# Kernel tuning notes

Hardware: AMD Instinct MI355X
Metric: run time of the kernel (lower is better)

## Reference

```python
import jax, jax.numpy as jnp
from jax import lax
import numpy as np

N = 17          # num_joints
HID = 64        # hidden_dim
EPS = 1e-5      # BatchNorm eps
SKELETON_CONNECTIONS = [(0, 1), (0, 2), (1, 3), (2, 4), (5, 7), (7, 9), (6, 8), (8, 10), (5, 6), (5, 11), (6, 12), (11, 13), (13, 15), (12, 14), (14, 16), (11, 12)]


def _build_adj():
    a = np.zeros((N, N), dtype=np.float32)
    np.fill_diagonal(a, 1.0)
    for i, j in SKELETON_CONNECTIONS:
        a[i, j] = 1.0
        a[j, i] = 1.0
    dinv = 1.0 / np.sqrt(a.sum(1))
    return jnp.asarray(a * dinv[:, None] * dinv[None, :])

ADJ = _build_adj()  # [N, N], D^-1/2 (A+I) D^-1/2


def _bn(x, g, b):
    # eval-mode BatchNorm1d with running_mean=0, running_var=1; x: [B, C, T]
    s = g / jnp.sqrt(1.0 + EPS)
    return x * s[None, :, None] + b[None, :, None]


def _gconv1d(x, w, b, groups, pad):
    # grouped temporal conv; x: [B, C, T], w: [Cout, Cin//groups, K]
    y = lax.conv_general_dilated(x, w, (1,), [(pad, pad)], feature_group_count=groups,
                                 dimension_numbers=('NCH', 'OIH', 'NCH'))
    return y + b[None, :, None]


def _block(x, gw, gb, bn1g, bn1b, cw, cb, bn2g, bn2b, res):
    # STGCNBlock; x: [B, T, N, Cin]
    B, T, n, Cin = x.shape
    Cout = gw.shape[1]
    xr = x.reshape(B, T, n * Cin).transpose(0, 2, 1)  # [B, n*Cin, T]
    if res is None:
        r = xr
    else:
        rw, rb, rg, rbb = res
        r = _bn(_gconv1d(xr, rw, rb, n, 0), rg, rbb)
    # GCN applied to all timesteps at once (replaces the per-t python loop):
    # support = x @ W ; out = adj @ support + bias
    y = jnp.einsum('mn,btno->btmo', ADJ, jnp.einsum('btni,io->btno', x, gw)) + gb
    h = y.reshape(B, T, n * Cout).transpose(0, 2, 1)  # [B, n*Cout, T]
    h = jax.nn.relu(_bn(h, bn1g, bn1b))
    h = _gconv1d(h, cw, cb, n, 1)                    # k=3, pad=1, groups=N
    h = jax.nn.relu(_bn(h, bn2g, bn2b))              # dropout is identity (eval)
    out = h + r
    return out.transpose(0, 2, 1).reshape(B, T, n, Cout)


def setup_inputs() -> dict:
    key = jax.random.key(0)
    ks = iter(jax.random.split(key, 64))

    def rn(shape, scale=0.05):
        return (scale * jax.random.normal(next(ks), shape)).astype(jnp.float32)

    B, T = 64, 512
    C = 2 * HID  # 128
    inp = {'x': jax.random.normal(next(ks), (B, T, N * 3), dtype=jnp.float32)}
    inp['w_in'] = rn((HID, 3))
    inp['b_in'] = rn((HID,))
    for i, cin in enumerate([HID, C, C]):
        inp[f'gw{i}'] = rn((cin, C))
        inp[f'gb{i}'] = rn((C,))
        inp[f'bn1g{i}'] = 1.0 + rn((N * C,))
        inp[f'bn1b{i}'] = rn((N * C,))
        inp[f'cw{i}'] = rn((N * C, C, 3))
        inp[f'cb{i}'] = rn((N * C,))
        inp[f'bn2g{i}'] = 1.0 + rn((N * C,))
        inp[f'bn2b{i}'] = rn((N * C,))
    inp['rw0'] = rn((N * C, HID, 1))
    inp['rb0'] = rn((N * C,))
    inp['rg0'] = 1.0 + rn((N * C,))
    inp['rbb0'] = rn((N * C,))
    inp['w1'] = rn((N * C, 128))
    inp['b1'] = rn((128,))
    inp['w2'] = rn((128, 64))
    inp['b2'] = rn((64,))
    inp['w3'] = rn((64, 1))
    inp['b3'] = rn((1,))
    return inp


def reference(x, w_in, b_in, gw0, gb0, bn1g0, bn1b0, cw0, cb0, bn2g0, bn2b0,
              gw1, gb1, bn1g1, bn1b1, cw1, cb1, bn2g1, bn2b1,
              gw2, gb2, bn1g2, bn1b2, cw2, cb2, bn2g2, bn2b2,
              rw0, rb0, rg0, rbb0, w1, b1, w2, b2, w3, b3):
    B, T, F = x.shape
    x4 = x.reshape(B, T, N, F // N)                       # [B,T,N,3]
    h = jnp.einsum('btnc,oc->btno', x4, w_in) + b_in      # Conv1d k=1 input transform
    h = _block(h, gw0, gb0, bn1g0, bn1b0, cw0, cb0, bn2g0, bn2b0, (rw0, rb0, rg0, rbb0))
    h = _block(h, gw1, gb1, bn1g1, bn1b1, cw1, cb1, bn2g1, bn2b1, None)
    h = _block(h, gw2, gb2, bn1g2, bn1b2, cw2, cb2, bn2g2, bn2b2, None)
    h = h.mean(axis=1).reshape(B, -1)                     # temporal mean -> [B, N*2*HID]
    h = jax.nn.relu(h @ w1 + b1)
    h = jax.nn.relu(h @ w2 + b2)
    return jax.nn.sigmoid(h @ w3 + b3)                    # [B, 1]
```

## Files before the change

kernel.cpp:

```cpp
#include <hip/hip_runtime.h>
#include <math.h>

#define BNUM 64
#define TNUM 512
#define NJ   17
#define CC   128
#define HIDC 64

#define RSQ 0.9999950000374997f

typedef __attribute__((ext_vector_type(8))) short bf16x8;
typedef __attribute__((ext_vector_type(4))) float f32x4;

__device__ __forceinline__ float bf2f(unsigned short u) {
    union { unsigned int i; float f; } v; v.i = ((unsigned int)u) << 16; return v.f;
}
__device__ __forceinline__ unsigned short f2bf(float f) {
    union { float f; unsigned int i; } v; v.f = f;
    return (unsigned short)((v.i + 0x7FFF + ((v.i >> 16) & 1)) >> 16);
}
__device__ __forceinline__ void unpack8(const uint4 v, float* f) {
    f[0] = bf2f((unsigned short)(v.x & 0xFFFF)); f[1] = bf2f((unsigned short)(v.x >> 16));
    f[2] = bf2f((unsigned short)(v.y & 0xFFFF)); f[3] = bf2f((unsigned short)(v.y >> 16));
    f[4] = bf2f((unsigned short)(v.z & 0xFFFF)); f[5] = bf2f((unsigned short)(v.z >> 16));
    f[6] = bf2f((unsigned short)(v.w & 0xFFFF)); f[7] = bf2f((unsigned short)(v.w >> 16));
}
__device__ __forceinline__ uint4 pack8(const float* f) {
    uint4 v;
    v.x = (unsigned)f2bf(f[0]) | ((unsigned)f2bf(f[1]) << 16);
    v.y = (unsigned)f2bf(f[2]) | ((unsigned)f2bf(f[3]) << 16);
    v.z = (unsigned)f2bf(f[4]) | ((unsigned)f2bf(f[5]) << 16);
    v.w = (unsigned)f2bf(f[6]) | ((unsigned)f2bf(f[7]) << 16);
    return v;
}

constexpr unsigned ADJM[NJ] = {
    0x7u, 0xBu, 0x15u, 0xAu, 0x14u,
    0x8E0u, 0x1160u, 0x2A0u, 0x540u, 0x280u, 0x500u,
    0x3820u, 0x5840u, 0xA800u, 0x15000u, 0xA000u, 0x14000u
};
constexpr float DINV[NJ] = {
    0.5773502691896258f, 0.5773502691896258f, 0.5773502691896258f,
    0.7071067811865476f, 0.7071067811865476f,
    0.5f, 0.5f,
    0.5773502691896258f, 0.5773502691896258f,
    0.7071067811865476f, 0.7071067811865476f,
    0.5f, 0.5f,
    0.5773502691896258f, 0.5773502691896258f,
    0.7071067811865476f, 0.7071067811865476f
};

__global__ void k_fallback(float* out) { out[threadIdx.x] = 0.f; }
__global__ void k_zero(float* p, int n) {
    const int i = blockIdx.x * 256 + threadIdx.x;
    if (i < n) p[i] = 0.f;
}

__global__ void k_prep_cwB(const float* __restrict__ cw0, const float* __restrict__ cw1,
                           const float* __restrict__ cw2, unsigned short* __restrict__ cwB) {
    const int idx = blockIdx.x * 256 + threadIdx.x;
    if (idx >= NJ * CC * 3 * CC) return;
    const float* cw = (blockIdx.y == 0) ? cw0 : (blockIdx.y == 1) ? cw1 : cw2;
    const int oc = idx / 384, kk = idx % 384;
    const int ktap = kk >> 7, i = kk & 127;
    cwB[(size_t)blockIdx.y * (NJ * CC * 3 * CC) + idx] =
        f2bf(cw[((size_t)oc * CC + i) * 3 + ktap]);
}
__global__ void k_prep_rwB(const float* __restrict__ rw, unsigned short* __restrict__ rwB) {
    const int idx = blockIdx.x * 256 + threadIdx.x;
    if (idx >= NJ * CC * HIDC) return;
    rwB[idx] = f2bf(rw[idx]);
}
template<int CIN>
__global__ void k_prep_gwB(const float* __restrict__ gw, unsigned short* __restrict__ gwB) {
    const int idx = blockIdx.x * 256 + threadIdx.x;
    if (idx >= CC * CIN) return;
    const int o = idx / CIN, i = idx % CIN;
    gwB[idx] = f2bf(gw[i * CC + o]);
}

template<int CIN>
__device__ __forceinline__ void gcn_mfma_body(
        const unsigned short* __restrict__ gwB,
        const float* __restrict__ gb,
        const float* __restrict__ bn1g, const float* __restrict__ bn1b,
        unsigned short* __restrict__ H1, unsigned short* lds,
        int bt0, int tid) {
    const int lane = tid & 63;
    const int wnt  = tid >> 6;
    const int rbase = lane & 15;
    const int g8    = (lane >> 4) * 8;

    f32x4 acc[17][2] = {};
#pragma unroll
    for (int ks = 0; ks < CIN / 32; ++ks) {
        bf16x8 bfr[2];
#pragma unroll
        for (int nt = 0; nt < 2; ++nt)
            bfr[nt] = *reinterpret_cast<const bf16x8*>(
                &gwB[(size_t)(wnt * 32 + nt * 16 + rbase) * CIN + ks * 32 + g8]);
#pragma unroll
        for (int mt = 0; mt < 17; ++mt) {
            const int rl = mt * 16 + rbase;
            const bf16x8 a = *reinterpret_cast<const bf16x8*>(
                &lds[(rl * CIN + ks * 32 + g8) ^ ((rl & 7) << 3)]);
            acc[mt][0] = __builtin_amdgcn_mfma_f32_16x16x32_bf16(a, bfr[0], acc[mt][0], 0, 0, 0);
            acc[mt][1] = __builtin_amdgcn_mfma_f32_16x16x32_bf16(a, bfr[1], acc[mt][1], 0, 0, 0);
        }
    }
    __syncthreads();

    const int rrow = (lane >> 4) * 4;
#pragma unroll
    for (int mt = 0; mt < 17; ++mt)
#pragma unroll
        for (int nt = 0; nt < 2; ++nt)
#pragma unroll
            for (int q = 0; q < 4; ++q) {
                const int r = mt * 16 + rrow + q;
                const int o = wnt * 32 + nt * 16 + rbase;
                lds[(r * 128 + o) ^ ((r & 7) << 3)] = f2bf(acc[mt][nt][q]);
            }
    __syncthreads();

    const int btl = tid >> 4;
    const int cg  = tid & 15;
    float s8[NJ][8];
#pragma unroll
    for (int n = 0; n < NJ; ++n) {
        const int r = btl * NJ + n;
        const uint4 raw = *reinterpret_cast<const uint4*>(
            &lds[(r * 128 + cg * 8) ^ ((r & 7) << 3)]);
        unpack8(raw, s8[n]);
    }
#pragma unroll
    for (int m = 0; m < NJ; ++m) {
        float ym[8] = {};
#pragma unroll
        for (int n = 0; n < NJ; ++n) {
            if (ADJM[m] & (1u << n)) {
#pragma unroll
                for (int j = 0; j < 8; ++j) ym[j] = fmaf(s8[n][j], DINV[n], ym[j]);
            }
        }
        const int ch0 = m * CC + cg * 8;
        const float4 g0 = *reinterpret_cast<const float4*>(&gb[ch0]);
        const float4 g1 = *reinterpret_cast<const float4*>(&gb[ch0 + 4]);
        const float4 a0 = *reinterpret_cast<const float4*>(&bn1g[ch0]);
        const float4 a1 = *reinterpret_cast<const float4*>(&bn1g[ch0 + 4]);
        const float4 c0 = *reinterpret_cast<const float4*>(&bn1b[ch0]);
        const float4 c1 = *reinterpret_cast<const float4*>(&bn1b[ch0 + 4]);
        const float gbv[8] = {g0.x, g0.y, g0.z, g0.w, g1.x, g1.y, g1.z, g1.w};
        const float sgv[8] = {a0.x, a0.y, a0.z, a0.w, a1.x, a1.y, a1.z, a1.w};
        const float sbv[8] = {c0.x, c0.y, c0.z, c0.w, c1.x, c1.y, c1.z, c1.w};
        float out8[8];
#pragma unroll
        for (int j = 0; j < 8; ++j) {
            const float y = fmaf(ym[j], DINV[m], gbv[j]);
            out8[j] = fmaxf(fmaf(y, sgv[j] * RSQ, sbv[j]), 0.f);
        }
        *reinterpret_cast<uint4*>(&H1[(size_t)(bt0 + btl) * (NJ * CC) + ch0]) = pack8(out8);
    }
}

__global__ __launch_bounds__(256, 1) void k_gcn_mfma(
        const unsigned short* __restrict__ X, const unsigned short* __restrict__ gwB,
        const float* __restrict__ gb,
        const float* __restrict__ bn1g, const float* __restrict__ bn1b,
        unsigned short* __restrict__ H1) {
    __shared__ __align__(16) unsigned short lds[272 * 128];
    const int bt0 = blockIdx.x * 16;
    const int tid = threadIdx.x;
    for (int c = tid; c < 272 * 16; c += 256) {
        const int rl = c >> 4, s8 = c & 15;
        const uint4 v = *reinterpret_cast<const uint4*>(
            &X[(size_t)(bt0 * NJ + rl) * CC + s8 * 8]);
        *reinterpret_cast<uint4*>(&lds[(rl * 128 + s8 * 8) ^ ((rl & 7) << 3)]) = v;
    }
    __syncthreads();
    gcn_mfma_body<CC>(gwB, gb, bn1g, bn1b, H1, lds, bt0, tid);
}

__global__ __launch_bounds__(256, 1) void k_gcn0_mfma(
        const float* __restrict__ x,
        const float* __restrict__ w_in, const float* __restrict__ b_in,
        const unsigned short* __restrict__ gwB,
        const float* __restrict__ gb,
        const float* __restrict__ bn1g, const float* __restrict__ bn1b,
        unsigned short* __restrict__ H1) {
    __shared__ __align__(16) unsigned short lds[272 * 128];
    const int bt0 = blockIdx.x * 16;
    const int tid = threadIdx.x;
    for (int c = tid; c < 272 * 8; c += 256) {
        const int rl = c >> 3, i8 = c & 7;
        const int bt = bt0 + rl / NJ, n = rl % NJ;
        const float* xb = &x[(size_t)bt * (NJ * 3) + n * 3];
        const float x0 = xb[0], x1 = xb[1], x2 = xb[2];
        unsigned short tmp[8];
#pragma unroll
        for (int jj = 0; jj < 8; ++jj) {
            const int i = i8 * 8 + jj;
            tmp[jj] = f2bf(fmaf(x2, w_in[i * 3 + 2],
                           fmaf(x1, w_in[i * 3 + 1],
                           fmaf(x0, w_in[i * 3 + 0], b_in[i]))));
        }
        *reinterpret_cast<uint4*>(&lds[(rl * HIDC + i8 * 8) ^ ((rl & 7) << 3)]) =
            *reinterpret_cast<uint4*>(tmp);
    }
    __syncthreads();
    gcn_mfma_body<HIDC>(gwB, gb, bn1g, bn1b, H1, lds, bt0, tid);
}

template<int RES_MODE, int POOL>
__global__ __launch_bounds__(256) void k_tconv_mfma(
        const unsigned short* __restrict__ H1, const unsigned short* __restrict__ cwB,
        const float* __restrict__ cb,
        const float* __restrict__ bn2g, const float* __restrict__ bn2b,
        const float* __restrict__ RSRC,
        const float* __restrict__ w_in, const float* __restrict__ b_in,
        const unsigned short* __restrict__ rwB, const float* __restrict__ rb,
        const float* __restrict__ rg, const float* __restrict__ rbb,
        unsigned short* __restrict__ OUT, float* __restrict__ pooled) {
    __shared__ __align__(16) unsigned short xin[66 * 128];
    __shared__ __align__(16) unsigned short h0s[RES_MODE ? 64 * 64 : 8];

    const int t0  = blockIdx.x * 64;
    const int n   = blockIdx.y;
    const int b   = blockIdx.z;
    const int tid = threadIdx.x;
    const int lane = tid & 63;
    const int wnt  = tid >> 6;

    for (int c = tid; c < 66 * 16; c += 256) {
        const int row = c >> 4, slot = c & 15;
        const int ti = t0 - 1 + row;
        uint4 v = {0u, 0u, 0u, 0u};
        if (ti >= 0 && ti < TNUM)
            v = *reinterpret_cast<const uint4*>(
                    &H1[(((size_t)b * TNUM + ti) * NJ + n) * CC + slot * 8]);
        const int u = (row * 128 + slot * 8) ^ ((row & 7) << 3);
        *reinterpret_cast<uint4*>(&xin[u]) = v;
    }
    if constexpr (RES_MODE == 1) {
        for (int c = tid; c < 64 * 8; c += 256) {
            const int r = c >> 3, i8 = c & 7;
            const float* xb = &RSRC[((size_t)b * TNUM + t0 + r) * (NJ * 3) + n * 3];
            const float x0 = xb[0], x1 = xb[1], x2 = xb[2];
            unsigned short tmp[8];
#pragma unroll
            for (int j = 0; j < 8; ++j) {
                const int i = i8 * 8 + j;
                tmp[j] = f2bf(fmaf(x2, w_in[i * 3 + 2],
                              fmaf(x1, w_in[i * 3 + 1],
                              fmaf(x0, w_in[i * 3 + 0], b_in[i]))));
            }
            const int u = (r * 64 + i8 * 8) ^ ((r & 7) << 3);
            *reinterpret_cast<uint4*>(&h0s[u]) = *reinterpret_cast<uint4*>(tmp);
        }
    }
    __syncthreads();

    const int rbase = lane & 15;
    const int g8    = (lane >> 4) * 8;

    f32x4 acc[4][2] = {};
    for (int ks = 0; ks < 12; ++ks) {
        const int ktap = ks >> 2;
        const int ib   = (ks & 3) * 32 + g8;
        bf16x8 a[4];
#pragma unroll
        for (int m = 0; m < 4; ++m) {
            const int rl = m * 16 + rbase + ktap;
            a[m] = *reinterpret_cast<const bf16x8*>(
                       &xin[(rl * 128 + ib) ^ ((rl & 7) << 3)]);
        }
#pragma unroll
        for (int nt = 0; nt < 2; ++nt) {
            const int o = wnt * 32 + nt * 16 + rbase;
            const bf16x8 bf = *reinterpret_cast<const bf16x8*>(
                &cwB[(size_t)(n * CC + o) * 384 + ks * 32 + g8]);
#pragma unroll
            for (int m = 0; m < 4; ++m)
                acc[m][nt] = __builtin_amdgcn_mfma_f32_16x16x32_bf16(a[m], bf, acc[m][nt], 0, 0, 0);
        }
    }

    f32x4 accr[4][2] = {};
    if constexpr (RES_MODE == 1) {
        for (int ks = 0; ks < 2; ++ks) {
            const int ib = ks * 32 + g8;
            bf16x8 a[4];
#pragma unroll
            for (int m = 0; m < 4; ++m) {
                const int rl = m * 16 + rbase;
                a[m] = *reinterpret_cast<const bf16x8*>(
                           &h0s[(rl * 64 + ib) ^ ((rl & 7) << 3)]);
            }
#pragma unroll
            for (int nt = 0; nt < 2; ++nt) {
                const int o = wnt * 32 + nt * 16 + rbase;
                const bf16x8 bf = *reinterpret_cast<const bf16x8*>(
                    &rwB[(size_t)(n * CC + o) * HIDC + ib]);
#pragma unroll
                for (int m = 0; m < 4; ++m)
                    accr[m][nt] = __builtin_amdgcn_mfma_f32_16x16x32_bf16(a[m], bf, accr[m][nt], 0, 0, 0);
            }
        }
    }

    __syncthreads();

    const int rrow = (lane >> 4) * 4;
#pragma unroll
    for (int nt = 0; nt < 2; ++nt) {
        const int o  = wnt * 32 + nt * 16 + rbase;
        const int ch = n * CC + o;
        const float s2 = bn2g[ch] * RSQ, bb2 = bn2b[ch], cbo = cb[ch];
        float rs = 0.f, rsh = 0.f, rbc = 0.f;
        if constexpr (RES_MODE == 1) { rs = rg[ch] * RSQ; rsh = rbb[ch]; rbc = rb[ch]; }
#pragma unroll
        for (int m = 0; m < 4; ++m) {
#pragma unroll
            for (int q = 0; q < 4; ++q) {
                const int r = m * 16 + rrow + q;
                float v = fmaxf(fmaf(acc[m][nt][q] + cbo, s2, bb2), 0.f);
                if constexpr (RES_MODE == 1) v += fmaf(accr[m][nt][q] + rbc, rs, rsh);
                xin[(r * 128 + o) ^ ((r & 7) << 3)] = f2bf(v);
            }
        }
    }
    __syncthreads();

    float pacc[8] = {};
    for (int c = tid; c < 64 * 16; c += 256) {
        const int r = c >> 4, s8 = c & 15;
        uint4 v = *reinterpret_cast<const uint4*>(
            &xin[(r * 128 + s8 * 8) ^ ((r & 7) << 3)]);
        const size_t oi = (((size_t)b * TNUM + t0 + r) * NJ + n) * CC + s8 * 8;
        if constexpr (RES_MODE == 0) {
            float f[8], g[8];
            unpack8(v, f);
            unpack8(*reinterpret_cast<const uint4*>(&OUT[oi]), g);
#pragma unroll
            for (int j = 0; j < 8; ++j) f[j] += g[j];
            if constexpr (POOL == 1) {
#pragma unroll
                for (int j = 0; j < 8; ++j) pacc[j] += f[j];
            } else {
                *reinterpret_cast<uint4*>(&OUT[oi]) = pack8(f);
            }
        } else {
            *reinterpret_cast<uint4*>(&OUT[oi]) = v;
        }
    }

    if constexpr (POOL == 1) {
        __syncthreads();
        float* fred = reinterpret_cast<float*>(xin);
#pragma unroll
        for (int j = 0; j < 8; ++j) fred[tid * 8 + j] = pacc[j];
        __syncthreads();
        if (tid < 128) {
            const int s8 = tid >> 3, j = tid & 7;
            float s = 0.f;
#pragma unroll
            for (int k = 0; k < 16; ++k) s += fred[(s8 + 16 * k) * 8 + j];
            atomicAdd(&pooled[((size_t)b * NJ + n) * CC + s8 * 8 + j], s * (1.0f / TNUM));
        }
    }
}

__global__ __launch_bounds__(128) void k_mlp(const float* __restrict__ P,
        const float* __restrict__ w1, const float* __restrict__ b1,
        const float* __restrict__ w2, const float* __restrict__ b2,
        const float* __restrict__ w3, const float* __restrict__ b3,
        float* __restrict__ out) {
    __shared__ float h1[128];
    __shared__ float h2[64];
    const int b = blockIdx.x, tid = threadIdx.x;
    const float* pr = P + (size_t)b * (NJ * CC);
    float acc = b1[tid];
    for (int i = 0; i < NJ * CC; ++i) acc = fmaf(pr[i], w1[i * 128 + tid], acc);
    h1[tid] = fmaxf(acc, 0.f);
    __syncthreads();
    if (tid < 64) {
        float a2 = b2[tid];
#pragma unroll 4
        for (int i = 0; i < 128; ++i) a2 = fmaf(h1[i], w2[i * 64 + tid], a2);
        h2[tid] = fmaxf(a2, 0.f);
    }
    __syncthreads();
    if (tid == 0) {
        float a3 = b3[0];
#pragma unroll 4
        for (int i = 0; i < 64; ++i) a3 = fmaf(h2[i], w3[i], a3);
        out[b] = 1.f / (1.f + expf(-a3));
    }
}

extern "C" void kernel_launch(void* const* d_in, const int* in_sizes, int n_in,
                              void* d_out, int out_size, void* d_ws, size_t ws_size,
                              hipStream_t stream) {
    const float* x    = (const float*)d_in[0];
    const float* w_in = (const float*)d_in[1];
    const float* b_in = (const float*)d_in[2];
    const float *gw[3], *gb[3], *bn1g[3], *bn1b[3], *cw[3], *cb[3], *bn2g[3], *bn2b[3];
    for (int l = 0; l < 3; ++l) {
        const int base = 3 + l * 8;
        gw[l]   = (const float*)d_in[base + 0];
        gb[l]   = (const float*)d_in[base + 1];
        bn1g[l] = (const float*)d_in[base + 2];
        bn1b[l] = (const float*)d_in[base + 3];
        cw[l]   = (const float*)d_in[base + 4];
        cb[l]   = (const float*)d_in[base + 5];
        bn2g[l] = (const float*)d_in[base + 6];
        bn2b[l] = (const float*)d_in[base + 7];
    }
    const float* rw0  = (const float*)d_in[27];
    const float* rb0  = (const float*)d_in[28];
    const float* rg0  = (const float*)d_in[29];
    const float* rbb0 = (const float*)d_in[30];
    const float* w1   = (const float*)d_in[31];
    const float* b1   = (const float*)d_in[32];
    const float* w2   = (const float*)d_in[33];
    const float* b2   = (const float*)d_in[34];
    const float* w3   = (const float*)d_in[35];
    const float* b3   = (const float*)d_in[36];

    const size_t CWB    = (size_t)NJ * CC * 3 * CC;
    const size_t RWB    = (size_t)NJ * CC * HIDC;
    const size_t GWB128 = (size_t)CC * CC;
    const size_t GWB64  = (size_t)CC * HIDC;
    const size_t ACT_B  = (size_t)TNUM * NJ * CC;
    const size_t POOLED = (size_t)BNUM * NJ * CC;
    const size_t fixedB = (3 * CWB + RWB + 2 * GWB128 + GWB64) * sizeof(unsigned short)
                        + POOLED * sizeof(float);

    int chunk = 0;
    for (int c = BNUM; c >= 1; c >>= 1) {
        const size_t need = fixedB + 2 * (size_t)c * ACT_B * sizeof(unsigned short);
        if (need <= ws_size) { chunk = c; break; }
    }
    if (chunk == 0) {
        k_fallback<<<1, 64, 0, stream>>>((float*)d_out);
        return;
    }

    unsigned short* cwB0 = (unsigned short*)d_ws;
    unsigned short* cwB1 = cwB0 + CWB;
    unsigned short* cwB2 = cwB1 + CWB;
    unsigned short* rwB  = cwB2 + CWB;
    unsigned short* gwB0 = rwB + RWB;
    unsigned short* gwB1 = gwB0 + GWB64;
    unsigned short* gwB2 = gwB1 + GWB128;
    float* pooled = (float*)(gwB2 + GWB128);
    unsigned short* bufA = (unsigned short*)(pooled + POOLED);
    unsigned short* bufB = bufA + (size_t)chunk * ACT_B;

    dim3 pgrid((int)((CWB + 255) / 256), 3, 1);
    k_prep_cwB<<<pgrid, 256, 0, stream>>>(cw[0], cw[1], cw[2], cwB0);
    k_prep_rwB<<<(int)((RWB + 255) / 256), 256, 0, stream>>>(rw0, rwB);
    k_prep_gwB<HIDC><<<(int)((GWB64 + 255) / 256), 256, 0, stream>>>(gw[0], gwB0);
    k_prep_gwB<CC><<<(int)((GWB128 + 255) / 256), 256, 0, stream>>>(gw[1], gwB1);
    k_prep_gwB<CC><<<(int)((GWB128 + 255) / 256), 256, 0, stream>>>(gw[2], gwB2);
    k_zero<<<(int)((POOLED + 255) / 256), 256, 0, stream>>>(pooled, (int)POOLED);

    for (int b0 = 0; b0 < BNUM; b0 += chunk) {
        const float* xc = x + (size_t)b0 * TNUM * NJ * 3;
        const int GB = chunk * TNUM / 16;
        const dim3 tgrid(TNUM / 64, NJ, chunk);
        float* pc = pooled + (size_t)b0 * NJ * CC;

        k_gcn0_mfma<<<GB, 256, 0, stream>>>(xc, w_in, b_in, gwB0,
                                            gb[0], bn1g[0], bn1b[0], bufA);
        k_tconv_mfma<1, 0><<<tgrid, 256, 0, stream>>>(bufA, cwB0, cb[0], bn2g[0], bn2b[0],
                                                      xc, w_in, b_in, rwB, rb0, rg0, rbb0,
                                                      bufB, nullptr);
        k_gcn_mfma<<<GB, 256, 0, stream>>>(bufB, gwB1, gb[1], bn1g[1], bn1b[1], bufA);
        k_tconv_mfma<0, 0><<<tgrid, 256, 0, stream>>>(bufA, cwB1, cb[1], bn2g[1], bn2b[1],
                                                      nullptr, w_in, b_in, nullptr, nullptr, nullptr, nullptr,
                                                      bufB, nullptr);
        k_gcn_mfma<<<GB, 256, 0, stream>>>(bufB, gwB2, gb[2], bn1g[2], bn1b[2], bufA);
        k_tconv_mfma<0, 1><<<tgrid, 256, 0, stream>>>(bufA, cwB2, cb[2], bn2g[2], bn2b[2],
                                                      nullptr, w_in, b_in, nullptr, nullptr, nullptr, nullptr,
                                                      bufB, pc);
    }

    k_mlp<<<BNUM, 128, 0, stream>>>(pooled, w1, b1, w2, b2, w3, b3, (float*)d_out);
}
```

Before: 1.038 ms.

## Loop temporal conv blocks over time with double-buffered LDS prefetch

The temporal conv kernel now launches one block per (joint, batch) and loops over all eight 64-step time tiles. The next tile is prefetched into registers and written to a second LDS buffer, which overlaps global loads with MFMA work. The epilogue writes output straight from accumulators instead of staging through LDS. Pooling now reduces in registers with wave shuffles and a plain store, so the atomics and the zeroing kernel go away. The weight-prep kernels are merged into one launch. Grid parallelism drops eightfold (17×chunk blocks), which risks low occupancy, and the element-wise bf16 global stores are less coalesced.

```diff
diff --git a/kernel.cpp b/kernel.cpp
--- a/kernel.cpp
+++ b/kernel.cpp
@@ -51,10 +51,6 @@
 };
 
 __global__ void k_fallback(float* out) { out[threadIdx.x] = 0.f; }
-__global__ void k_zero(float* p, int n) {
-    const int i = blockIdx.x * 256 + threadIdx.x;
-    if (i < n) p[i] = 0.f;
-}
 
 __global__ void k_prep_cwB(const float* __restrict__ cw0, const float* __restrict__ cw1,
                            const float* __restrict__ cw2, unsigned short* __restrict__ cwB) {
@@ -66,17 +62,22 @@
     cwB[(size_t)blockIdx.y * (NJ * CC * 3 * CC) + idx] =
         f2bf(cw[((size_t)oc * CC + i) * 3 + ktap]);
 }
-__global__ void k_prep_rwB(const float* __restrict__ rw, unsigned short* __restrict__ rwB) {
-    const int idx = blockIdx.x * 256 + threadIdx.x;
-    if (idx >= NJ * CC * HIDC) return;
-    rwB[idx] = f2bf(rw[idx]);
-}
-template<int CIN>
-__global__ void k_prep_gwB(const float* __restrict__ gw, unsigned short* __restrict__ gwB) {
-    const int idx = blockIdx.x * 256 + threadIdx.x;
-    if (idx >= CC * CIN) return;
-    const int o = idx / CIN, i = idx % CIN;
-    gwB[idx] = f2bf(gw[i * CC + o]);
+__global__ void k_prep_misc(const float* __restrict__ rw,
+                            const float* __restrict__ gw0, const float* __restrict__ gw1,
+                            const float* __restrict__ gw2,
+                            unsigned short* __restrict__ rwB, unsigned short* __restrict__ gwB0,
+                            unsigned short* __restrict__ gwB1, unsigned short* __restrict__ gwB2) {
+    int idx = blockIdx.x * 256 + threadIdx.x;
+    if (idx < NJ * CC * HIDC) { rwB[idx] = f2bf(rw[idx]); return; }
+    idx -= NJ * CC * HIDC;
+    if (idx < CC * HIDC) { const int o = idx / HIDC, i = idx % HIDC;
+        gwB0[idx] = f2bf(gw0[i * CC + o]); return; }
+    idx -= CC * HIDC;
+    if (idx < CC * CC) { const int o = idx / CC, i = idx % CC;
+        gwB1[idx] = f2bf(gw1[i * CC + o]); return; }
+    idx -= CC * CC;
+    if (idx < CC * CC) { const int o = idx / CC, i = idx % CC;
+        gwB2[idx] = f2bf(gw2[i * CC + o]); return; }
 }
 
 template<int CIN>
@@ -221,151 +222,178 @@
         const unsigned short* __restrict__ rwB, const float* __restrict__ rb,
         const float* __restrict__ rg, const float* __restrict__ rbb,
         unsigned short* __restrict__ OUT, float* __restrict__ pooled) {
-    __shared__ __align__(16) unsigned short xin[66 * 128];
-    __shared__ __align__(16) unsigned short h0s[RES_MODE ? 64 * 64 : 8];
-
-    const int t0  = blockIdx.x * 64;
-    const int n   = blockIdx.y;
-    const int b   = blockIdx.z;
+    __shared__ __align__(16) unsigned short xin[2][66 * 128];
+    __shared__ __align__(16) unsigned short h0s[RES_MODE ? 2 : 1][RES_MODE ? 64 * 64 : 8];
+
+    const int n   = blockIdx.x;
+    const int b   = blockIdx.y;
     const int tid = threadIdx.x;
     const int lane = tid & 63;
     const int wnt  = tid >> 6;
 
-    for (int c = tid; c < 66 * 16; c += 256) {
-        const int row = c >> 4, slot = c & 15;
-        const int ti = t0 - 1 + row;
-        uint4 v = {0u, 0u, 0u, 0u};
-        if (ti >= 0 && ti < TNUM)
-            v = *reinterpret_cast<const uint4*>(
-                    &H1[(((size_t)b * TNUM + ti) * NJ + n) * CC + slot * 8]);
-        const int u = (row * 128 + slot * 8) ^ ((row & 7) << 3);
-        *reinterpret_cast<uint4*>(&xin[u]) = v;
-    }
-    if constexpr (RES_MODE == 1) {
-        for (int c = tid; c < 64 * 8; c += 256) {
-            const int r = c >> 3, i8 = c & 7;
-            const float* xb = &RSRC[((size_t)b * TNUM + t0 + r) * (NJ * 3) + n * 3];
-            const float x0 = xb[0], x1 = xb[1], x2 = xb[2];
-            unsigned short tmp[8];
-#pragma unroll
-            for (int j = 0; j < 8; ++j) {
-                const int i = i8 * 8 + j;
-                tmp[j] = f2bf(fmaf(x2, w_in[i * 3 + 2],
-                              fmaf(x1, w_in[i * 3 + 1],
-                              fmaf(x0, w_in[i * 3 + 0], b_in[i]))));
-            }
-            const int u = (r * 64 + i8 * 8) ^ ((r & 7) << 3);
-            *reinterpret_cast<uint4*>(&h0s[u]) = *reinterpret_cast<uint4*>(tmp);
-        }
-    }
-    __syncthreads();
+    uint4 sreg[5];
+    float hx[2][3];
+
+    auto LOADT = [&](int it) {
+        const int t0 = it * 64;
+#pragma unroll
+        for (int j = 0; j < 5; ++j) {
+            const int c = tid + 256 * j;
+            if (c < 66 * 16) {
+                const int row = c >> 4, slot = c & 15;
+                const int ti = t0 - 1 + row;
+                uint4 v = {0u, 0u, 0u, 0u};
+                if (ti >= 0 && ti < TNUM)
+                    v = *reinterpret_cast<const uint4*>(
+                            &H1[(((size_t)b * TNUM + ti) * NJ + n) * CC + slot * 8]);
+                sreg[j] = v;
+            }
+        }
+    };
+    auto WRITET = [&](int buf) {
+#pragma unroll
+        for (int j = 0; j < 5; ++j) {
+            const int c = tid + 256 * j;
+            if (c < 66 * 16) {
+                const int row = c >> 4, slot = c & 15;
+                *reinterpret_cast<uint4*>(&xin[buf][(row * 128 + slot * 8) ^ ((row & 7) << 3)]) = sreg[j];
+            }
+        }
+    };
+    auto LOADH = [&](int it) {
+        if constexpr (RES_MODE == 1) {
+            const int t0 = it * 64;
+#pragma unroll
+            for (int j = 0; j < 2; ++j) {
+                const int c = tid + 256 * j;
+                const int r = c >> 3;
+                const float* xb = &RSRC[((size_t)b * TNUM + t0 + r) * (NJ * 3) + n * 3];
+                hx[j][0] = xb[0]; hx[j][1] = xb[1]; hx[j][2] = xb[2];
+            }
+        }
+    };
+    auto WRITEH = [&](int buf) {
+        if constexpr (RES_MODE == 1) {
+#pragma unroll
+            for (int j = 0; j < 2; ++j) {
+                const int c = tid + 256 * j;
+                const int r = c >> 3, i8 = c & 7;
+                float f[8];
+#pragma unroll
+                for (int jj = 0; jj < 8; ++jj) {
+                    const int i = i8 * 8 + jj;
+                    f[jj] = fmaf(hx[j][2], w_in[i * 3 + 2],
+                            fmaf(hx[j][1], w_in[i * 3 + 1],
+                            fmaf(hx[j][0], w_in[i * 3 + 0], b_in[i])));
+                }
+                *reinterpret_cast<uint4*>(&h0s[buf][(r * 64 + i8 * 8) ^ ((r & 7) << 3)]) = pack8(f);
+            }
+        }
+    };
 
     const int rbase = lane & 15;
     const int g8    = (lane >> 4) * 8;
-
-    f32x4 acc[4][2] = {};
-    for (int ks = 0; ks < 12; ++ks) {
-        const int ktap = ks >> 2;
-        const int ib   = (ks & 3) * 32 + g8;
-        bf16x8 a[4];
-#pragma unroll
-        for (int m = 0; m < 4; ++m) {
-            const int rl = m * 16 + rbase + ktap;
-            a[m] = *reinterpret_cast<const bf16x8*>(
-                       &xin[(rl * 128 + ib) ^ ((rl & 7) << 3)]);
-        }
-#pragma unroll
-        for (int nt = 0; nt < 2; ++nt) {
-            const int o = wnt * 32 + nt * 16 + rbase;
-            const bf16x8 bf = *reinterpret_cast<const bf16x8*>(
-                &cwB[(size_t)(n * CC + o) * 384 + ks * 32 + g8]);
-#pragma unroll
-            for (int m = 0; m < 4; ++m)
-                acc[m][nt] = __builtin_amdgcn_mfma_f32_16x16x32_bf16(a[m], bf, acc[m][nt], 0, 0, 0);
-        }
-    }
-
-    f32x4 accr[4][2] = {};
-    if constexpr (RES_MODE == 1) {
-        for (int ks = 0; ks < 2; ++ks) {
-            const int ib = ks * 32 + g8;
+    const int rrow  = (lane >> 4) * 4;
+
+    float s2[2], bb2v[2], cbov[2], rsv[2], rshv[2], rbcv[2];
+#pragma unroll
+    for (int nt = 0; nt < 2; ++nt) {
+        const int ch = n * CC + wnt * 32 + nt * 16 + rbase;
+        s2[nt] = bn2g[ch] * RSQ; bb2v[nt] = bn2b[ch]; cbov[nt] = cb[ch];
+        if constexpr (RES_MODE == 1) { rsv[nt] = rg[ch] * RSQ; rshv[nt] = rbb[ch]; rbcv[nt] = rb[ch]; }
+        else { rsv[nt] = rshv[nt] = rbcv[nt] = 0.f; }
+    }
+
+    float pacc[2] = {0.f, 0.f};
+
+    LOADT(0); LOADH(0);
+    WRITET(0); WRITEH(0);
+    LOADT(1); LOADH(1);
+    __syncthreads();
+
+    for (int it = 0; it < 8; ++it) {
+        const int cur = it & 1, nxt = cur ^ 1;
+        const int t0 = it * 64;
+
+        f32x4 acc[4][2] = {};
+        for (int ks = 0; ks < 12; ++ks) {
+            const int ktap = ks >> 2;
+            const int ib   = (ks & 3) * 32 + g8;
             bf16x8 a[4];
 #pragma unroll
             for (int m = 0; m < 4; ++m) {
-                const int rl = m * 16 + rbase;
+                const int rl = m * 16 + rbase + ktap;
                 a[m] = *reinterpret_cast<const bf16x8*>(
-                           &h0s[(rl * 64 + ib) ^ ((rl & 7) << 3)]);
+                           &xin[cur][(rl * 128 + ib) ^ ((rl & 7) << 3)]);
             }
 #pragma unroll
             for (int nt = 0; nt < 2; ++nt) {
                 const int o = wnt * 32 + nt * 16 + rbase;
                 const bf16x8 bf = *reinterpret_cast<const bf16x8*>(
-                    &rwB[(size_t)(n * CC + o) * HIDC + ib]);
+                    &cwB[(size_t)(n * CC + o) * 384 + ks * 32 + g8]);
 #pragma unroll
                 for (int m = 0; m < 4; ++m)
-                    accr[m][nt] = __builtin_amdgcn_mfma_f32_16x16x32_bf16(a[m], bf, accr[m][nt], 0, 0, 0);
-            }
-        }
-    }
-
-    __syncthreads();
-
-    const int rrow = (lane >> 4) * 4;
-#pragma unroll
-    for (int nt = 0; nt < 2; ++nt) {
-        const int o  = wnt * 32 + nt * 16 + rbase;
-        const int ch = n * CC + o;
-        const float s2 = bn2g[ch] * RSQ, bb2 = bn2b[ch], cbo = cb[ch];
-        float rs = 0.f, rsh = 0.f, rbc = 0.f;
-        if constexpr (RES_MODE == 1) { rs = rg[ch] * RSQ; rsh = rbb[ch]; rbc = rb[ch]; }
-#pragma unroll
-        for (int m = 0; m < 4; ++m) {
-#pragma unroll
-            for (int q = 0; q < 4; ++q) {
-                const int r = m * 16 + rrow + q;
-                float v = fmaxf(fmaf(acc[m][nt][q] + cbo, s2, bb2), 0.f);
-                if constexpr (RES_MODE == 1) v += fmaf(accr[m][nt][q] + rbc, rs, rsh);
-                xin[(r * 128 + o) ^ ((r & 7) << 3)] = f2bf(v);
-            }
-        }
-    }
-    __syncthreads();
-
-    float pacc[8] = {};
-    for (int c = tid; c < 64 * 16; c += 256) {
-        const int r = c >> 4, s8 = c & 15;
-        uint4 v = *reinterpret_cast<const uint4*>(
-            &xin[(r * 128 + s8 * 8) ^ ((r & 7) << 3)]);
-        const size_t oi = (((size_t)b * TNUM + t0 + r) * NJ + n) * CC + s8 * 8;
-        if constexpr (RES_MODE == 0) {
-            float f[8], g[8];
-            unpack8(v, f);
-            unpack8(*reinterpret_cast<const uint4*>(&OUT[oi]), g);
-#pragma unroll
-            for (int j = 0; j < 8; ++j) f[j] += g[j];
-            if constexpr (POOL == 1) {
-#pragma unroll
-                for (int j = 0; j < 8; ++j) pacc[j] += f[j];
-            } else {
-                *reinterpret_cast<uint4*>(&OUT[oi]) = pack8(f);
-            }
-        } else {
-            *reinterpret_cast<uint4*>(&OUT[oi]) = v;
-        }
+                    acc[m][nt] = __builtin_amdgcn_mfma_f32_16x16x32_bf16(a[m], bf, acc[m][nt], 0, 0, 0);
+            }
+        }
+
+        f32x4 accr[4][2] = {};
+        if constexpr (RES_MODE == 1) {
+            for (int ks = 0; ks < 2; ++ks) {
+                const int ib = ks * 32 + g8;
+                bf16x8 a[4];
+#pragma unroll
+                for (int m = 0; m < 4; ++m) {
+                    const int rl = m * 16 + rbase;
+                    a[m] = *reinterpret_cast<const bf16x8*>(
+                               &h0s[cur][(rl * 64 + ib) ^ ((rl & 7) << 3)]);
+                }
+#pragma unroll
+                for (int nt = 0; nt < 2; ++nt) {
+                    const int o = wnt * 32 + nt * 16 + rbase;
+                    const bf16x8 bf = *reinterpret_cast<const bf16x8*>(
+                        &rwB[(size_t)(n * CC + o) * HIDC + ib]);
+#pragma unroll
+                    for (int m = 0; m < 4; ++m)
+                        accr[m][nt] = __builtin_amdgcn_mfma_f32_16x16x32_bf16(a[m], bf, accr[m][nt], 0, 0, 0);
+                }
+            }
+        }
+
+#pragma unroll
+        for (int nt = 0; nt < 2; ++nt) {
+            const int o = wnt * 32 + nt * 16 + rbase;
+#pragma unroll
+            for (int m = 0; m < 4; ++m) {
+#pragma unroll
+                for (int q = 0; q < 4; ++q) {
+                    const int r = m * 16 + rrow + q;
+                    const size_t oi = (((size_t)b * TNUM + t0 + r) * NJ + n) * CC + o;
+                    float v = fmaxf(fmaf(acc[m][nt][q] + cbov[nt], s2[nt], bb2v[nt]), 0.f);
+                    if constexpr (RES_MODE == 1) v += fmaf(accr[m][nt][q] + rbcv[nt], rsv[nt], rshv[nt]);
+                    else                         v += bf2f(OUT[oi]);
+                    if constexpr (POOL == 1) pacc[nt] += v;
+                    else                     OUT[oi] = f2bf(v);
+                }
+            }
+        }
+
+        if (it < 7) { WRITET(nxt); WRITEH(nxt); }
+        if (it < 6) { LOADT(it + 2); LOADH(it + 2); }
+        __syncthreads();
     }
 
     if constexpr (POOL == 1) {
-        __syncthreads();
-        float* fred = reinterpret_cast<float*>(xin);
-#pragma unroll
-        for (int j = 0; j < 8; ++j) fred[tid * 8 + j] = pacc[j];
-        __syncthreads();
-        if (tid < 128) {
-            const int s8 = tid >> 3, j = tid & 7;
-            float s = 0.f;
-#pragma unroll
-            for (int k = 0; k < 16; ++k) s += fred[(s8 + 16 * k) * 8 + j];
-            atomicAdd(&pooled[((size_t)b * NJ + n) * CC + s8 * 8 + j], s * (1.0f / TNUM));
+#pragma unroll
+        for (int nt = 0; nt < 2; ++nt) {
+            pacc[nt] += __shfl_xor(pacc[nt], 16);
+            pacc[nt] += __shfl_xor(pacc[nt], 32);
+        }
+        if ((lane >> 4) == 0) {
+#pragma unroll
+            for (int nt = 0; nt < 2; ++nt)
+                pooled[((size_t)b * NJ + n) * CC + wnt * 32 + nt * 16 + rbase] =
+                    pacc[nt] * (1.0f / TNUM);
         }
     }
 }
@@ -459,16 +487,14 @@
 
     dim3 pgrid((int)((CWB + 255) / 256), 3, 1);
     k_prep_cwB<<<pgrid, 256, 0, stream>>>(cw[0], cw[1], cw[2], cwB0);
-    k_prep_rwB<<<(int)((RWB + 255) / 256), 256, 0, stream>>>(rw0, rwB);
-    k_prep_gwB<HIDC><<<(int)((GWB64 + 255) / 256), 256, 0, stream>>>(gw[0], gwB0);
-    k_prep_gwB<CC><<<(int)((GWB128 + 255) / 256), 256, 0, stream>>>(gw[1], gwB1);
-    k_prep_gwB<CC><<<(int)((GWB128 + 255) / 256), 256, 0, stream>>>(gw[2], gwB2);
-    k_zero<<<(int)((POOLED + 255) / 256), 256, 0, stream>>>(pooled, (int)POOLED);
+    const size_t MISC = RWB + GWB64 + 2 * GWB128;
+    k_prep_misc<<<(int)((MISC + 255) / 256), 256, 0, stream>>>(
+        rw0, gw[0], gw[1], gw[2], rwB, gwB0, gwB1, gwB2);
 
     for (int b0 = 0; b0 < BNUM; b0 += chunk) {
         const float* xc = x + (size_t)b0 * TNUM * NJ * 3;
         const int GB = chunk * TNUM / 16;
-        const dim3 tgrid(TNUM / 64, NJ, chunk);
+        const dim3 tgrid(NJ, chunk);
         float* pc = pooled + (size_t)b0 * NJ * CC;
 
         k_gcn0_mfma<<<GB, 256, 0, stream>>>(xc, w_in, b_in, gwB0,
```

New measurement: 1.242 ms. 19.6% more time.

## Reorder GCN tile rows joint-major to apply adjacency in registers

Applied to the files above, without the earlier changes.

The GCN kernels now load each block's rows joint-major (row = joint*16 + timestep) instead of timestep-major. Each MFMA M-tile then corresponds to one joint across 16 timesteps, so the adjacency mixing runs directly on accumulator registers. This removes the LDS write-back, two barriers and the reload/unpack stage. The trade-off is that output stores become scattered 2-byte writes instead of 16-byte vector stores. Separately, the four small weight-prep kernels are merged into one launch, and the tconv K loops get unroll pragmas.

```diff
diff --git a/kernel.cpp b/kernel.cpp
--- a/kernel.cpp
+++ b/kernel.cpp
@@ -66,17 +66,22 @@
     cwB[(size_t)blockIdx.y * (NJ * CC * 3 * CC) + idx] =
         f2bf(cw[((size_t)oc * CC + i) * 3 + ktap]);
 }
-__global__ void k_prep_rwB(const float* __restrict__ rw, unsigned short* __restrict__ rwB) {
-    const int idx = blockIdx.x * 256 + threadIdx.x;
-    if (idx >= NJ * CC * HIDC) return;
-    rwB[idx] = f2bf(rw[idx]);
-}
-template<int CIN>
-__global__ void k_prep_gwB(const float* __restrict__ gw, unsigned short* __restrict__ gwB) {
-    const int idx = blockIdx.x * 256 + threadIdx.x;
-    if (idx >= CC * CIN) return;
-    const int o = idx / CIN, i = idx % CIN;
-    gwB[idx] = f2bf(gw[i * CC + o]);
+__global__ void k_prep_misc(const float* __restrict__ rw,
+                            const float* __restrict__ gw0, const float* __restrict__ gw1,
+                            const float* __restrict__ gw2,
+                            unsigned short* __restrict__ rwB, unsigned short* __restrict__ gwB0,
+                            unsigned short* __restrict__ gwB1, unsigned short* __restrict__ gwB2) {
+    int idx = blockIdx.x * 256 + threadIdx.x;
+    if (idx < NJ * CC * HIDC) { rwB[idx] = f2bf(rw[idx]); return; }
+    idx -= NJ * CC * HIDC;
+    if (idx < CC * HIDC) { const int o = idx / HIDC, i = idx % HIDC;
+        gwB0[idx] = f2bf(gw0[i * CC + o]); return; }
+    idx -= CC * HIDC;
+    if (idx < CC * CC) { const int o = idx / CC, i = idx % CC;
+        gwB1[idx] = f2bf(gw1[i * CC + o]); return; }
+    idx -= CC * CC;
+    if (idx < CC * CC) { const int o = idx / CC, i = idx % CC;
+        gwB2[idx] = f2bf(gw2[i * CC + o]); return; }
 }
 
 template<int CIN>
@@ -90,6 +95,7 @@
     const int wnt  = tid >> 6;
     const int rbase = lane & 15;
     const int g8    = (lane >> 4) * 8;
+    const int rrow  = (lane >> 4) * 4;
 
     f32x4 acc[17][2] = {};
 #pragma unroll
@@ -108,58 +114,41 @@
             acc[mt][1] = __builtin_amdgcn_mfma_f32_16x16x32_bf16(a, bfr[1], acc[mt][1], 0, 0, 0);
         }
     }
-    __syncthreads();
-
-    const int rrow = (lane >> 4) * 4;
-#pragma unroll
-    for (int mt = 0; mt < 17; ++mt)
+
+#pragma unroll
+    for (int n = 0; n < NJ; ++n)
 #pragma unroll
         for (int nt = 0; nt < 2; ++nt)
 #pragma unroll
-            for (int q = 0; q < 4; ++q) {
-                const int r = mt * 16 + rrow + q;
-                const int o = wnt * 32 + nt * 16 + rbase;
-                lds[(r * 128 + o) ^ ((r & 7) << 3)] = f2bf(acc[mt][nt][q]);
-            }
-    __syncthreads();
-
-    const int btl = tid >> 4;
-    const int cg  = tid & 15;
-    float s8[NJ][8];
-#pragma unroll
-    for (int n = 0; n < NJ; ++n) {
-        const int r = btl * NJ + n;
-        const uint4 raw = *reinterpret_cast<const uint4*>(
-            &lds[(r * 128 + cg * 8) ^ ((r & 7) << 3)]);
-        unpack8(raw, s8[n]);
-    }
+            for (int q = 0; q < 4; ++q)
+                acc[n][nt][q] *= DINV[n];
+
 #pragma unroll
     for (int m = 0; m < NJ; ++m) {
-        float ym[8] = {};
+        float ym[2][4] = {};
 #pragma unroll
         for (int n = 0; n < NJ; ++n) {
             if (ADJM[m] & (1u << n)) {
 #pragma unroll
-                for (int j = 0; j < 8; ++j) ym[j] = fmaf(s8[n][j], DINV[n], ym[j]);
-            }
-        }
-        const int ch0 = m * CC + cg * 8;
-        const float4 g0 = *reinterpret_cast<const float4*>(&gb[ch0]);
-        const float4 g1 = *reinterpret_cast<const float4*>(&gb[ch0 + 4]);
-        const float4 a0 = *reinterpret_cast<const float4*>(&bn1g[ch0]);
-        const float4 a1 = *reinterpret_cast<const float4*>(&bn1g[ch0 + 4]);
-        const float4 c0 = *reinterpret_cast<const float4*>(&bn1b[ch0]);
-        const float4 c1 = *reinterpret_cast<const float4*>(&bn1b[ch0 + 4]);
-        const float gbv[8] = {g0.x, g0.y, g0.z, g0.w, g1.x, g1.y, g1.z, g1.w};
-        const float sgv[8] = {a0.x, a0.y, a0.z, a0.w, a1.x, a1.y, a1.z, a1.w};
-        const float sbv[8] = {c0.x, c0.y, c0.z, c0.w, c1.x, c1.y, c1.z, c1.w};
-        float out8[8];
-#pragma unroll
-        for (int j = 0; j < 8; ++j) {
-            const float y = fmaf(ym[j], DINV[m], gbv[j]);
-            out8[j] = fmaxf(fmaf(y, sgv[j] * RSQ, sbv[j]), 0.f);
-        }
-        *reinterpret_cast<uint4*>(&H1[(size_t)(bt0 + btl) * (NJ * CC) + ch0]) = pack8(out8);
+                for (int nt = 0; nt < 2; ++nt)
+#pragma unroll
+                    for (int q = 0; q < 4; ++q)
+                        ym[nt][q] += acc[n][nt][q];
+            }
+        }
+#pragma unroll
+        for (int nt = 0; nt < 2; ++nt) {
+            const int o  = wnt * 32 + nt * 16 + rbase;
+            const int ch = m * CC + o;
+            const float sg = bn1g[ch] * RSQ, sb = bn1b[ch], gbo = gb[ch];
+#pragma unroll
+            for (int q = 0; q < 4; ++q) {
+                const int btl = rrow + q;
+                const float y = fmaf(ym[nt][q], DINV[m], gbo);
+                H1[((size_t)(bt0 + btl) * NJ + m) * CC + o] =
+                    f2bf(fmaxf(fmaf(y, sg, sb), 0.f));
+            }
+        }
     }
 }
 
@@ -173,8 +162,9 @@
     const int tid = threadIdx.x;
     for (int c = tid; c < 272 * 16; c += 256) {
         const int rl = c >> 4, s8 = c & 15;
+        const int n = rl >> 4, btl = rl & 15;
         const uint4 v = *reinterpret_cast<const uint4*>(
-            &X[(size_t)(bt0 * NJ + rl) * CC + s8 * 8]);
+            &X[((size_t)(bt0 + btl) * NJ + n) * CC + s8 * 8]);
         *reinterpret_cast<uint4*>(&lds[(rl * 128 + s8 * 8) ^ ((rl & 7) << 3)]) = v;
     }
     __syncthreads();
@@ -188,13 +178,13 @@
         const float* __restrict__ gb,
         const float* __restrict__ bn1g, const float* __restrict__ bn1b,
         unsigned short* __restrict__ H1) {
-    __shared__ __align__(16) unsigned short lds[272 * 128];
+    __shared__ __align__(16) unsigned short lds[272 * 64];
     const int bt0 = blockIdx.x * 16;
     const int tid = threadIdx.x;
     for (int c = tid; c < 272 * 8; c += 256) {
         const int rl = c >> 3, i8 = c & 7;
-        const int bt = bt0 + rl / NJ, n = rl % NJ;
-        const float* xb = &x[(size_t)bt * (NJ * 3) + n * 3];
+        const int n = rl >> 4, btl = rl & 15;
+        const float* xb = &x[(size_t)(bt0 + btl) * (NJ * 3) + n * 3];
         const float x0 = xb[0], x1 = xb[1], x2 = xb[2];
         unsigned short tmp[8];
 #pragma unroll
@@ -264,6 +254,7 @@
     const int g8    = (lane >> 4) * 8;
 
     f32x4 acc[4][2] = {};
+#pragma unroll
     for (int ks = 0; ks < 12; ++ks) {
         const int ktap = ks >> 2;
         const int ib   = (ks & 3) * 32 + g8;
@@ -287,6 +278,7 @@
 
     f32x4 accr[4][2] = {};
     if constexpr (RES_MODE == 1) {
+#pragma unroll
         for (int ks = 0; ks < 2; ++ks) {
             const int ib = ks * 32 + g8;
             bf16x8 a[4];
@@ -459,10 +451,9 @@
 
     dim3 pgrid((int)((CWB + 255) / 256), 3, 1);
     k_prep_cwB<<<pgrid, 256, 0, stream>>>(cw[0], cw[1], cw[2], cwB0);
-    k_prep_rwB<<<(int)((RWB + 255) / 256), 256, 0, stream>>>(rw0, rwB);
-    k_prep_gwB<HIDC><<<(int)((GWB64 + 255) / 256), 256, 0, stream>>>(gw[0], gwB0);
-    k_prep_gwB<CC><<<(int)((GWB128 + 255) / 256), 256, 0, stream>>>(gw[1], gwB1);
-    k_prep_gwB<CC><<<(int)((GWB128 + 255) / 256), 256, 0, stream>>>(gw[2], gwB2);
+    const size_t MISC = RWB + GWB64 + 2 * GWB128;
+    k_prep_misc<<<(int)((MISC + 255) / 256), 256, 0, stream>>>(
+        rw0, gw[0], gw[1], gw[2], rwB, gwB0, gwB1, gwB2);
     k_zero<<<(int)((POOLED + 255) / 256), 256, 0, stream>>>(pooled, (int)POOLED);
 
     for (int b0 = 0; b0 < BNUM; b0 += chunk) {
```

Measured after the change: 948.1 us. 8.7% less time.
